# Optimization experiments

Measured on AMD Instinct MI355X. Metric: run time of the kernel, lower is better.

The kernel has to match this reference:

```python
import jax, jax.numpy as jnp
import numpy as np

BIG_NEG = -1e9


def setup_inputs() -> dict:
    key = jax.random.key(0)
    ks = jax.random.split(key, 6)
    b, N1, d, C1, K = 4, 511, 64, 31, 32
    features = jax.random.normal(ks[0], (b, N1, d), jnp.float32)
    transition_logits = jax.random.normal(ks[1], (C1, C1), jnp.float32)
    init_logits = jax.random.uniform(ks[2], (C1,), jnp.float32)
    poisson_log_rates = jax.random.normal(ks[3], (C1,), jnp.float32) * 0.5 + 1.5
    A = jax.random.normal(ks[5], (d, d), jnp.float32)
    gaussian_cov = jnp.eye(d, dtype=jnp.float32) + 0.1 * (A @ A.T) / d
    gaussian_means = jax.random.normal(ks[4], (C1, d), jnp.float32) * 0.1
    return {
        "features": features,
        "transition_logits": transition_logits,
        "init_logits": init_logits,
        "poisson_log_rates": poisson_log_rates,
        "gaussian_means": gaussian_means,
        "gaussian_cov": gaussian_cov,
        "max_k": K,
        "add_eos": 1,
    }


def reference(features, transition_logits, init_logits, poisson_log_rates,
              gaussian_means, gaussian_cov, max_k, add_eos):
    b, N1, d = features.shape
    C1 = transition_logits.shape[0]
    K = int(max_k)
    dt = features.dtype

    # transition log-probs: mask diagonal with BIG_NEG, normalize over axis 0 (torch dim=0)
    trans = jax.nn.log_softmax(
        jnp.where(jnp.eye(C1, dtype=bool), jnp.asarray(BIG_NEG, dt), transition_logits), axis=0)
    init = jax.nn.log_softmax(init_logits)

    # Poisson duration log-probs: k*log(rate) - rate - lgamma(k+1), k = 0..K-1
    rates = jnp.exp(poisson_log_rates)  # [C1]
    tsteps = jnp.arange(K, dtype=dt)[:, None]  # [K,1]
    length = tsteps * poisson_log_rates[None, :] - rates[None, :] - jax.scipy.special.gammaln(tsteps + 1.0)  # [K,C1]

    # Gaussian emission log-probs, shared full covariance across classes
    L = jnp.linalg.cholesky(gaussian_cov)
    Linv = jax.scipy.linalg.solve_triangular(L, jnp.eye(d, dtype=dt), lower=True)
    diff = features[:, :, None, :] - gaussian_means[None, None]          # [b,N1,C1,d]
    y = jnp.einsum('bncd,ed->bnce', diff, Linv)
    maha = jnp.sum(y * y, axis=-1)                                       # [b,N1,C1]
    logdet = 2.0 * jnp.sum(jnp.log(jnp.diag(L)))
    emis = -0.5 * (d * jnp.log(jnp.asarray(2.0 * jnp.pi, dt)) + logdet + maha)

    if add_eos:
        N, C = N1 + 1, C1 + 1
        trans_a = jnp.full((C, C), BIG_NEG, dt).at[:C1, :C1].set(trans).at[C1, :].set(0.0)
        init_a = jnp.full((C,), BIG_NEG, dt).at[:C1].set(init)
        length_a = jnp.full((K, C), BIG_NEG, dt).at[:, :C1].set(length).at[1, C1].set(0.0)
        emis_a = jnp.full((b, N, C), BIG_NEG, dt).at[:, :N1, :C1].set(emis).at[:, N1, C1].set(0.0)
    else:
        N, C = N1, C1
        trans_a, init_a, length_a, emis_a = trans, init, length, emis

    ep = jnp.pad(emis_a, ((0, 0), (0, K), (0, 0)))
    cs = jnp.concatenate([jnp.zeros((b, 1, C), dt), jnp.cumsum(ep, axis=1)], axis=1)  # [b,N+K+1,C]
    tt = jnp.arange(N - 1)[:, None]
    kk = jnp.arange(K)[None, :]
    win = cs[:, tt + kk] - cs[:, tt]  # [b, N-1, K, C]

    # edge scores: b x (N-1) x K x C_prev x C
    scores = (trans_a[None, None, None] +
              length_a[None, None, :, None, :] +
              win[:, :, :, None, :])
    scores = scores.at[:, 0].add(init_a[None, None, None, :])
    keos = jnp.arange(1, K)
    scores = scores.at[:, N - 1 - keos, keos].add(emis_a[:, N - 1][:, None, :, None])
    return scores
```

## Files before the change

kernel.cpp:

```cpp
#include <hip/hip_runtime.h>
#include <math.h>

#define BIG_NEG -1.0e9f

typedef float f4 __attribute__((ext_vector_type(4)));

constexpr int B  = 4;
constexpr int N1 = 511;
constexpr int C1 = 31;
constexpr int K  = 32;
constexpr int N  = N1 + 1;
constexpr int C  = C1 + 1;

constexpr int WS_TRANS = 0;
constexpr int WS_INIT  = 1024;
constexpr int WS_LEN   = 1056;
constexpr int WS_P     = 2080;
constexpr int WS_W     = 6176;
constexpr int WS_BIAS  = 8224;
constexpr int WS_EMIS  = 8256;

__global__ __launch_bounds__(512) void k_prep(const float* __restrict__ tl,
                                              const float* __restrict__ il,
                                              const float* __restrict__ plr,
                                              const float* __restrict__ cov,
                                              const float* __restrict__ means,
                                              float* __restrict__ ws) {
    __shared__ float M[64][132];
    __shared__ float cP[2][4][64];
    __shared__ float Bsave[16][16];
    __shared__ float mu[C1][64];

    const int tid = threadIdx.x;
    const int ii = tid >> 3;
    const int cg = tid & 7;

    f4* Mrow = (f4*)&M[ii][0];

    for (int idx = tid; idx < 1024; idx += 512) {
        const int i = idx >> 5, j = idx & 31;
        float lv;
        if (j < C1) {
            float lr = plr[j];
            lv = (float)i * lr - expf(lr) - lgammaf((float)i + 1.0f);
        } else {
            lv = (i == 1) ? 0.0f : BIG_NEG;
        }
        ws[WS_LEN + idx] = lv;
        if (i == C1) ws[WS_TRANS + idx] = 0.0f;
        else if (j == C1) ws[WS_TRANS + idx] = BIG_NEG;
    }
    if (tid < B * C) {
        const int bb = tid >> 5, cc = tid & 31;
        ws[WS_EMIS + (bb * N + N1) * C + cc] = (cc == C1) ? 0.0f : BIG_NEG;
    }
    if (tid < C1) {
        const int jj = tid;
        float m = BIG_NEG;
        for (int r = 0; r < C1; ++r) {
            float v = (r == jj) ? BIG_NEG : tl[r * C1 + jj];
            m = fmaxf(m, v);
        }
        float s = 0.0f;
        for (int r = 0; r < C1; ++r) {
            float v = (r == jj) ? BIG_NEG : tl[r * C1 + jj];
            s += expf(v - m);
        }
        float lse = m + logf(s);
        for (int r = 0; r < C1; ++r) {
            float v = (r == jj) ? BIG_NEG : tl[r * C1 + jj];
            ws[WS_TRANS + r * 32 + jj] = v - lse;
        }
    }
    if (tid == 32) {
        float m = -1.0e30f;
        for (int cc = 0; cc < C1; ++cc) m = fmaxf(m, il[cc]);
        float s = 0.0f;
        for (int cc = 0; cc < C1; ++cc) s += expf(il[cc] - m);
        float lse = m + logf(s);
        for (int cc = 0; cc < C1; ++cc) ws[WS_INIT + cc] = il[cc] - lse;
        ws[WS_INIT + C1] = BIG_NEG;
    }

    {
        Mrow[cg]     = *(const f4*)&cov[ii * 64 + 4 * cg];
        Mrow[cg + 8] = *(const f4*)&cov[ii * 64 + 4 * (cg + 8)];
        const int r0 = 4 * cg, r1 = 4 * (cg + 8);
        f4 e1 = {(ii == r0) ? 1.f : 0.f, (ii == r0 + 1) ? 1.f : 0.f,
                 (ii == r0 + 2) ? 1.f : 0.f, (ii == r0 + 3) ? 1.f : 0.f};
        f4 e2 = {(ii == r1) ? 1.f : 0.f, (ii == r1 + 1) ? 1.f : 0.f,
                 (ii == r1 + 2) ? 1.f : 0.f, (ii == r1 + 3) ? 1.f : 0.f};
        Mrow[cg + 16] = e1;
        Mrow[cg + 24] = e2;
    }
    if (cg == 0) {
        cP[0][0][ii] = cov[ii * 64 + 0];
        cP[0][1][ii] = cov[ii * 64 + 1];
        cP[0][2][ii] = cov[ii * 64 + 2];
        cP[0][3][ii] = cov[ii * 64 + 3];
    }
    for (int idx = tid; idx < C1 * 64; idx += 512)
        mu[idx >> 6][idx & 63] = means[idx];
    __syncthreads();

    float detprod = 1.0f;
    for (int st = 0; st < 16; ++st) {
        const int s = st << 2;
        const int par = st & 1;
        const float T00 = cP[par][0][s + 0], T01 = cP[par][0][s + 1],
                    T02 = cP[par][0][s + 2], T03 = cP[par][0][s + 3];
        const float T10 = cP[par][1][s + 0], T11 = cP[par][1][s + 1],
                    T12 = cP[par][1][s + 2], T13 = cP[par][1][s + 3];
        const float T20 = cP[par][2][s + 0], T21 = cP[par][2][s + 1],
                    T22 = cP[par][2][s + 2], T23 = cP[par][2][s + 3];
        const float T30 = cP[par][3][s + 0], T31 = cP[par][3][s + 1],
                    T32 = cP[par][3][s + 2], T33 = cP[par][3][s + 3];
        const float r0 = __builtin_amdgcn_rcpf(T00);
        const float l10 = T10 * r0, l20 = T20 * r0, l30 = T30 * r0;
        const float u11 = T11 - l10 * T01, u12 = T12 - l10 * T02,
                    u13 = T13 - l10 * T03;
        const float r1 = __builtin_amdgcn_rcpf(u11);
        const float l21 = (T21 - l20 * T01) * r1;
        const float l31 = (T31 - l30 * T01) * r1;
        const float u22 = T22 - l20 * T02 - l21 * u12;
        const float u23 = T23 - l20 * T03 - l21 * u13;
        const float u32 = T32 - l30 * T02 - l31 * u12;
        const float u33t = T33 - l30 * T03 - l31 * u13;
        const float r2 = __builtin_amdgcn_rcpf(u22);
        const float l32 = u32 * r2;
        const float u33 = u33t - l32 * u23;
        const float r3 = __builtin_amdgcn_rcpf(u33);
        detprod *= T00 * u11 * u22 * u33;

        if (tid < 16) Bsave[st][tid] = cP[par][tid & 3][s + (tid >> 2)];

        const float m0 = cP[par][0][ii], m1 = cP[par][1][ii],
                    m2 = cP[par][2][ii], m3 = cP[par][3][ii];
        const float y0 = m0;
        const float y1 = m1 - l10 * y0;
        const float y2 = m2 - l20 * y0 - l21 * y1;
        const float y3 = m3 - l30 * y0 - l31 * y1 - l32 * y2;
        float g3 = y3 * r3;
        float g2 = (y2 - u23 * g3) * r2;
        float g1 = (y1 - u12 * g2 - u13 * g3) * r1;
        float g0 = (y0 - T01 * g1 - T02 * g2 - T03 * g3) * r0;
        const bool pivrow = (unsigned)(ii - s) < 4u;
        if (pivrow) { g0 = 0.f; g1 = 0.f; g2 = 0.f; g3 = 0.f; }

        const f4* Ms0 = (const f4*)&M[s + 0][0];
        const f4* Ms1 = (const f4*)&M[s + 1][0];
        const f4* Ms2 = (const f4*)&M[s + 2][0];
        const f4* Ms3 = (const f4*)&M[s + 3][0];
        const int qpub = st + 1;
#pragma unroll
        for (int h = 0; h < 4; ++h) {
            const int q = cg + 8 * h;
            const int k0 = 4 * q;
            const bool active = (k0 < 64) ? (k0 + 3 >= s) : (k0 - 64 <= s + 3);
            if (!active) continue;
            f4 v = Mrow[q] - g0 * Ms0[q] - g1 * Ms1[q]
                           - g2 * Ms2[q] - g3 * Ms3[q];
            if (!pivrow) Mrow[q] = v;
            if (st < 15 && q == qpub) {
                cP[par ^ 1][0][ii] = v.x;
                cP[par ^ 1][1][ii] = v.y;
                cP[par ^ 1][2][ii] = v.z;
                cP[par ^ 1][3][ii] = v.w;
            }
        }
        __syncthreads();
    }

    {
        const int kb = ii >> 2, rsel = ii & 3, base = kb << 2;
        const float* Bk = &Bsave[kb][0];
        const float T00 = Bk[0],  T01 = Bk[4],  T02 = Bk[8],  T03 = Bk[12];
        const float T10 = Bk[1],  T11 = Bk[5],  T12 = Bk[9],  T13 = Bk[13];
        const float T20 = Bk[2],  T21 = Bk[6],  T22 = Bk[10], T23 = Bk[14];
        const float T30 = Bk[3],  T31 = Bk[7],  T32 = Bk[11], T33 = Bk[15];
        const float r0 = __builtin_amdgcn_rcpf(T00);
        const float l10 = T10 * r0, l20 = T20 * r0, l30 = T30 * r0;
        const float u11 = T11 - l10 * T01, u12 = T12 - l10 * T02,
                    u13 = T13 - l10 * T03;
        const float r1 = __builtin_amdgcn_rcpf(u11);
        const float l21 = (T21 - l20 * T01) * r1;
        const float l31 = (T31 - l30 * T01) * r1;
        const float u22 = T22 - l20 * T02 - l21 * u12;
        const float u23 = T23 - l20 * T03 - l21 * u13;
        const float u32 = T32 - l30 * T02 - l31 * u12;
        const float u33t = T33 - l30 * T03 - l31 * u13;
        const float r2 = __builtin_amdgcn_rcpf(u22);
        const float l32 = u32 * r2;
        const float u33 = u33t - l32 * u23;
        const float r3 = __builtin_amdgcn_rcpf(u33);
        const float m0 = (rsel == 0) ? 1.f : 0.f;
        const float m1 = (rsel == 1) ? 1.f : 0.f;
        const float m2 = (rsel == 2) ? 1.f : 0.f;
        const float m3 = (rsel == 3) ? 1.f : 0.f;
        const float y0 = m0;
        const float y1 = m1 - l10 * y0;
        const float y2 = m2 - l20 * y0 - l21 * y1;
        const float y3 = m3 - l30 * y0 - l31 * y1 - l32 * y2;
        const float x3 = y3 * r3;
        const float x2 = (y2 - u23 * x3) * r2;
        const float x1 = (y1 - u12 * x2 - u13 * x3) * r1;
        const float x0 = (y0 - T01 * x1 - T02 * x2 - T03 * x3) * r0;

        const f4* R0 = (const f4*)&M[base + 0][64];
        const f4* R1 = (const f4*)&M[base + 1][64];
        const f4* R2 = (const f4*)&M[base + 2][64];
        const f4* R3 = (const f4*)&M[base + 3][64];
        f4 va = x0 * R0[cg] + x1 * R1[cg] + x2 * R2[cg] + x3 * R3[cg];
        f4 vb = x0 * R0[cg + 8] + x1 * R1[cg + 8] +
                x2 * R2[cg + 8] + x3 * R3[cg + 8];
        *(f4*)&ws[WS_P + ii * 64 + 4 * cg] = va;
        *(f4*)&ws[WS_P + ii * 64 + 32 + 4 * cg] = vb;
        *(f4*)&M[ii][4 * cg] = va;
        *(f4*)&M[ii][32 + 4 * cg] = vb;
    }
    __syncthreads();

    {
        const int c = tid >> 4;
        const int l = tid & 15;
        if (c < C1) {
            const f4* muc = (const f4*)&mu[c][0];
            float qacc = 0.0f;
#pragma unroll
            for (int h = 0; h < 4; ++h) {
                const int dd = l + 16 * h;
                const f4* Mr = (const f4*)&M[dd][0];
                f4 a4 = {0.f, 0.f, 0.f, 0.f};
#pragma unroll
                for (int e4 = 0; e4 < 16; ++e4) a4 += Mr[e4] * muc[e4];
                float a = (a4.x + a4.y) + (a4.z + a4.w);
                ws[WS_W + dd * 32 + c] = a;
                qacc += a * mu[c][dd];
            }
            for (int m2 = 8; m2 >= 1; m2 >>= 1) qacc += __shfl_xor(qacc, m2, 64);
            if (l == 0)
                ws[WS_BIAS + c] = -0.5f * (64.0f * 1.8378770664093453f +
                                           logf(detprod) + qacc);
        }
    }
}

__global__ __launch_bounds__(256) void k_emis(const float* __restrict__ feat,
                                              float* __restrict__ ws) {
    const int tid = threadIdx.x;
    const int w = tid >> 6, lane = tid & 63;
    const int flat = blockIdx.x * 4 + w;
    const int b = flat / N1, n = flat % N1;
    __shared__ float xs[4][64];

    const float x = feat[flat * 64 + lane];
    xs[w][lane] = x;

    const float* __restrict__ P = ws + WS_P;
    float z = 0.0f;
    for (int dd = 0; dd < 64; ++dd) z += P[dd * 64 + lane] * xs[w][dd];

    float xz = x * z;
    for (int m = 32; m >= 1; m >>= 1) xz += __shfl_xor(xz, m);

    float val = BIG_NEG;
    if (lane < C1) {
        float s = ws[WS_BIAS + lane] - 0.5f * xz;
        const float* __restrict__ wT = ws + WS_W;
        for (int dd = 0; dd < 64; ++dd) s += wT[dd * 32 + lane] * xs[w][dd];
        val = s;
    }
    if (lane < C) ws[WS_EMIS + (b * N + n) * C + lane] = val;
}

__global__ __launch_bounds__(256) void k_main(const float* __restrict__ ws,
                                              float* __restrict__ out) {
    const int bid = blockIdx.x;
    const int b = bid / N1, t = bid % N1;
    const int tid = threadIdx.x;
    __shared__ float sh[32][36];

    {
        const int row = tid >> 3;
        const int c4 = (tid & 7) << 2;
        f4 v = {0.f, 0.f, 0.f, 0.f};
        if (t + row < N)
            v = *(const f4*)&ws[WS_EMIS + (b * N + t + row) * C + c4];
        *(f4*)&sh[row][c4] = v;
    }
    __syncthreads();

    {
        const int sc = tid >> 3;
        const int g  = tid & 7;
        float p0 = sh[4 * g + 0][sc];
        float p1 = p0 + sh[4 * g + 1][sc];
        float p2 = p1 + sh[4 * g + 2][sc];
        float p3 = p2 + sh[4 * g + 3][sc];
        float sum = p3;
#pragma unroll
        for (int off = 1; off < 8; off <<= 1) {
            float nv = __shfl_up(sum, off, 8);
            if (g >= off) sum += nv;
        }
        const float excl = sum - p3;
        sh[4 * g + 0][sc] = p0 + excl;
        sh[4 * g + 1][sc] = p1 + excl;
        sh[4 * g + 2][sc] = p2 + excl;
        sh[4 * g + 3][sc] = p3 + excl;
    }

    const int cp = tid >> 3;
    const int c0 = (tid & 7) << 2;
    f4 pre = *(const f4*)&ws[WS_TRANS + cp * 32 + c0];
    if (t == 0) {
        f4 in4 = *(const f4*)&ws[WS_INIT + c0];
        pre = pre + in4;
    }
    const float emisN = (cp == C1) ? 0.0f : BIG_NEG;
    const int keos = N1 - t;
    const size_t obase = (size_t)bid * (K * C * C) + (size_t)(cp * 32 + c0);
    __syncthreads();

#pragma unroll 4
    for (int k = 0; k < K; ++k) {
        f4 len4 = *(const f4*)&ws[WS_LEN + k * 32 + c0];
        f4 w4 = {0.f, 0.f, 0.f, 0.f};
        if (k > 0) w4 = *(const f4*)&sh[k - 1][c0];
        f4 o = pre + len4 + w4;
        if (k == keos) o = o + emisN;
        *(f4*)&out[obase + (size_t)k * (C * C)] = o;
    }
}

extern "C" void kernel_launch(void* const* d_in, const int* in_sizes, int n_in,
                              void* d_out, int out_size, void* d_ws, size_t ws_size,
                              hipStream_t stream) {
    const float* feat = (const float*)d_in[0];
    const float* tl   = (const float*)d_in[1];
    const float* il   = (const float*)d_in[2];
    const float* plr  = (const float*)d_in[3];
    const float* gm   = (const float*)d_in[4];
    const float* gc   = (const float*)d_in[5];
    float* ws  = (float*)d_ws;
    float* out = (float*)d_out;

    hipLaunchKernelGGL(k_prep, dim3(1), dim3(512), 0, stream, tl, il, plr, gc, gm, ws);
    hipLaunchKernelGGL(k_emis, dim3(B * N1 / 4), dim3(256), 0, stream, feat, ws);
    hipLaunchKernelGGL(k_main, dim3(B * N1), dim3(256), 0, stream, ws, out);
}
```

Baseline: 79.98 us.

## Fuse emission computation into main kernel with 8-timestep tiles per block

Drops the separate emission kernel and its workspace round trip. Each block now handles 8 consecutive timesteps: it loads the precision matrix and weights into shared memory, computes emissions for the 38 rows it needs, prefix-sums them, and writes the windowed score tensors for all 8 timesteps. This removes one launch and the global emission buffer, and amortizes the prefix scan across timesteps. In exchange it recomputes emissions for overlapping rows between blocks and shrinks the grid from 2044 to 256 blocks, which may reduce parallelism for the write-bound output phase.

Measured after the change: 88.11 us. +10.2%, slower.

```diff
diff --git a/kernel.cpp b/kernel.cpp
--- a/kernel.cpp
+++ b/kernel.cpp
@@ -18,7 +18,6 @@
 constexpr int WS_P     = 2080;
 constexpr int WS_W     = 6176;
 constexpr int WS_BIAS  = 8224;
-constexpr int WS_EMIS  = 8256;
 
 __global__ __launch_bounds__(512) void k_prep(const float* __restrict__ tl,
                                               const float* __restrict__ il,
@@ -49,10 +48,6 @@
         ws[WS_LEN + idx] = lv;
         if (i == C1) ws[WS_TRANS + idx] = 0.0f;
         else if (j == C1) ws[WS_TRANS + idx] = BIG_NEG;
-    }
-    if (tid < B * C) {
-        const int bb = tid >> 5, cc = tid & 31;
-        ws[WS_EMIS + (bb * N + N1) * C + cc] = (cc == C1) ? 0.0f : BIG_NEG;
     }
     if (tid < C1) {
         const int jj = tid;
@@ -245,91 +240,112 @@
     }
 }
 
-__global__ __launch_bounds__(256) void k_emis(const float* __restrict__ feat,
-                                              float* __restrict__ ws) {
+__global__ __launch_bounds__(256) void k_main(const float* __restrict__ feat,
+                                              const float* __restrict__ ws,
+                                              float* __restrict__ out) {
+    constexpr int TT = 8;
+    constexpr int ROWS = TT - 1 + 31;
+    const int bid = blockIdx.x;
+    const int b = bid >> 6;
+    const int t0 = (bid & 63) << 3;
     const int tid = threadIdx.x;
     const int w = tid >> 6, lane = tid & 63;
-    const int flat = blockIdx.x * 4 + w;
-    const int b = flat / N1, n = flat % N1;
-    __shared__ float xs[4][64];
-
-    const float x = feat[flat * 64 + lane];
-    xs[w][lane] = x;
-
-    const float* __restrict__ P = ws + WS_P;
-    float z = 0.0f;
-    for (int dd = 0; dd < 64; ++dd) z += P[dd * 64 + lane] * xs[w][dd];
-
-    float xz = x * z;
-    for (int m = 32; m >= 1; m >>= 1) xz += __shfl_xor(xz, m);
-
-    float val = BIG_NEG;
-    if (lane < C1) {
-        float s = ws[WS_BIAS + lane] - 0.5f * xz;
-        const float* __restrict__ wT = ws + WS_W;
-        for (int dd = 0; dd < 64; ++dd) s += wT[dd * 32 + lane] * xs[w][dd];
-        val = s;
-    }
-    if (lane < C) ws[WS_EMIS + (b * N + n) * C + lane] = val;
-}
-
-__global__ __launch_bounds__(256) void k_main(const float* __restrict__ ws,
-                                              float* __restrict__ out) {
-    const int bid = blockIdx.x;
-    const int b = bid / N1, t = bid % N1;
-    const int tid = threadIdx.x;
-    __shared__ float sh[32][36];
-
-    {
-        const int row = tid >> 3;
-        const int c4 = (tid & 7) << 2;
-        f4 v = {0.f, 0.f, 0.f, 0.f};
-        if (t + row < N)
-            v = *(const f4*)&ws[WS_EMIS + (b * N + t + row) * C + c4];
-        *(f4*)&sh[row][c4] = v;
+
+    __shared__ float sP[64][64];
+    __shared__ float sW[64][32];
+    __shared__ float sx[ROWS][64];
+    __shared__ float sh[ROWS + 3][36];
+    __shared__ float sb[32];
+
+    {
+        float* p = &sP[0][0];
+        for (int i = tid; i < 1024; i += 256)
+            *(f4*)&p[4 * i] = *(const f4*)&ws[WS_P + 4 * i];
+        float* q = &sW[0][0];
+        for (int i = tid; i < 512; i += 256)
+            *(f4*)&q[4 * i] = *(const f4*)&ws[WS_W + 4 * i];
+        if (tid < 32) { sb[tid] = ws[WS_BIAS + tid]; sh[0][tid] = 0.f; }
+        else if (tid < 64) sh[ROWS + 1][tid - 32] = 0.f;
+        else if (tid < 96) sh[ROWS + 2][tid - 64] = 0.f;
+        for (int idx = tid; idx < ROWS * 16; idx += 256) {
+            const int row = idx >> 4, c4 = (idx & 15) << 2;
+            const int n = t0 + row;
+            f4 v = {0.f, 0.f, 0.f, 0.f};
+            if (n < N1) v = *(const f4*)&feat[(b * N1 + n) * 64 + c4];
+            *(f4*)&sx[row][c4] = v;
+        }
+    }
+    __syncthreads();
+
+    const float bias_l = (lane < C1) ? sb[lane] : 0.f;
+    for (int r = w; r < ROWS; r += 4) {
+        const int n = t0 + r;
+        float val;
+        if (n < N1) {
+            const float xl = sx[r][lane];
+            float z = 0.f, wv = 0.f;
+            for (int dd = 0; dd < 64; ++dd) {
+                const float xd = sx[r][dd];
+                z  += sP[dd][lane] * xd;
+                wv += sW[dd][lane & 31] * xd;
+            }
+            float xz = xl * z;
+            for (int m2 = 32; m2 >= 1; m2 >>= 1) xz += __shfl_xor(xz, m2);
+            val = (lane < C1) ? (bias_l + wv - 0.5f * xz) : BIG_NEG;
+        } else if (n == N1) {
+            val = (lane == C1) ? 0.0f : BIG_NEG;
+        } else {
+            val = 0.0f;
+        }
+        if (lane < 32) sh[r + 1][lane] = val;
     }
     __syncthreads();
 
     {
         const int sc = tid >> 3;
         const int g  = tid & 7;
-        float p0 = sh[4 * g + 0][sc];
-        float p1 = p0 + sh[4 * g + 1][sc];
-        float p2 = p1 + sh[4 * g + 2][sc];
-        float p3 = p2 + sh[4 * g + 3][sc];
-        float sum = p3;
+        float p0 = sh[5 * g + 1][sc];
+        float p1 = p0 + sh[5 * g + 2][sc];
+        float p2 = p1 + sh[5 * g + 3][sc];
+        float p3 = p2 + sh[5 * g + 4][sc];
+        float p4 = p3 + sh[5 * g + 5][sc];
+        float sum = p4;
 #pragma unroll
         for (int off = 1; off < 8; off <<= 1) {
             float nv = __shfl_up(sum, off, 8);
             if (g >= off) sum += nv;
         }
-        const float excl = sum - p3;
-        sh[4 * g + 0][sc] = p0 + excl;
-        sh[4 * g + 1][sc] = p1 + excl;
-        sh[4 * g + 2][sc] = p2 + excl;
-        sh[4 * g + 3][sc] = p3 + excl;
-    }
+        const float excl = sum - p4;
+        sh[5 * g + 1][sc] = p0 + excl;
+        sh[5 * g + 2][sc] = p1 + excl;
+        sh[5 * g + 3][sc] = p2 + excl;
+        sh[5 * g + 4][sc] = p3 + excl;
+        sh[5 * g + 5][sc] = p4 + excl;
+    }
+    __syncthreads();
 
     const int cp = tid >> 3;
     const int c0 = (tid & 7) << 2;
-    f4 pre = *(const f4*)&ws[WS_TRANS + cp * 32 + c0];
-    if (t == 0) {
-        f4 in4 = *(const f4*)&ws[WS_INIT + c0];
-        pre = pre + in4;
-    }
+    const f4 tr4 = *(const f4*)&ws[WS_TRANS + cp * 32 + c0];
     const float emisN = (cp == C1) ? 0.0f : BIG_NEG;
-    const int keos = N1 - t;
-    const size_t obase = (size_t)bid * (K * C * C) + (size_t)(cp * 32 + c0);
-    __syncthreads();
-
+
+    for (int j = 0; j < TT; ++j) {
+        const int t = t0 + j;
+        if (t >= N1) break;
+        f4 base_j = tr4;
+        if (t == 0) base_j += *(const f4*)&ws[WS_INIT + c0];
+        const f4 Sj = *(const f4*)&sh[j][c0];
+        const int keos = N1 - t;
+        const size_t obase =
+            (size_t)(b * N1 + t) * 32768 + (size_t)(cp * 32 + c0);
 #pragma unroll 4
-    for (int k = 0; k < K; ++k) {
-        f4 len4 = *(const f4*)&ws[WS_LEN + k * 32 + c0];
-        f4 w4 = {0.f, 0.f, 0.f, 0.f};
-        if (k > 0) w4 = *(const f4*)&sh[k - 1][c0];
-        f4 o = pre + len4 + w4;
-        if (k == keos) o = o + emisN;
-        *(f4*)&out[obase + (size_t)k * (C * C)] = o;
+        for (int k = 0; k < K; ++k) {
+            const f4 len4 = *(const f4*)&ws[WS_LEN + k * 32 + c0];
+            const f4 win = *(const f4*)&sh[j + k][c0] - Sj;
+            f4 o = base_j + len4 + win;
+            if (k == keos) o += emisN;
+            *(f4*)&out[obase + (size_t)k * 1024] = o;
+        }
     }
 }
 
@@ -346,6 +362,5 @@
     float* out = (float*)d_out;
 
     hipLaunchKernelGGL(k_prep, dim3(1), dim3(512), 0, stream, tl, il, plr, gc, gm, ws);
-    hipLaunchKernelGGL(k_emis, dim3(B * N1 / 4), dim3(256), 0, stream, feat, ws);
-    hipLaunchKernelGGL(k_main, dim3(B * N1), dim3(256), 0, stream, ws, out);
+    hipLaunchKernelGGL(k_main, dim3(B * 64), dim3(256), 0, stream, feat, ws, out);
 }
```

## Process two time steps per block using shared prefix sums and cached length table

Applied to the files above, without the earlier changes.

Each k_main block now handles two consecutive time steps. It builds one inclusive prefix sum over 33 emission rows plus a zero row, and forms window sums as differences of prefix entries. The length table is staged into shared memory instead of being read from global memory on every k iteration. Halving the grid and reusing the loaded emission rows is meant to cut per-block setup and redundant global loads. The cost is a larger shared footprint and a slightly longer serial scan per block. The kernel is dominated by the output write, which is unchanged.

After: 79.57 us. About the same (-0.5%).

```diff
diff --git a/kernel.cpp b/kernel.cpp
--- a/kernel.cpp
+++ b/kernel.cpp
@@ -275,61 +275,82 @@
 
 __global__ __launch_bounds__(256) void k_main(const float* __restrict__ ws,
                                               float* __restrict__ out) {
+    constexpr int TT = 2;
+    constexpr int EROWS = TT - 1 + 31;
     const int bid = blockIdx.x;
-    const int b = bid / N1, t = bid % N1;
+    const int b = bid >> 8;
+    const int t0 = (bid & 255) << 1;
     const int tid = threadIdx.x;
-    __shared__ float sh[32][36];
-
-    {
-        const int row = tid >> 3;
-        const int c4 = (tid & 7) << 2;
+
+    __shared__ __align__(16) float slen[K * C];
+    __shared__ float sh[41][36];
+
+    for (int idx = tid; idx < K * C / 4; idx += 256)
+        *(f4*)&slen[4 * idx] = *(const f4*)&ws[WS_LEN + 4 * idx];
+
+    for (int idx = tid; idx < 33 * 8; idx += 256) {
+        const int r = idx >> 3, c4 = (idx & 7) << 2;
+        const int n = t0 + r;
         f4 v = {0.f, 0.f, 0.f, 0.f};
-        if (t + row < N)
-            v = *(const f4*)&ws[WS_EMIS + (b * N + t + row) * C + c4];
-        *(f4*)&sh[row][c4] = v;
-    }
+        if (n < N) v = *(const f4*)&ws[WS_EMIS + (b * N + n) * C + c4];
+        *(f4*)&sh[r + 1][c4] = v;
+    }
+    if (tid < 32) sh[0][tid] = 0.f;
+    if (tid >= 64 && tid < 288 - 32) {
+        const int z = tid - 64;
+        sh[34 + (z >> 5)][z & 31] = 0.f;
+    }
+    if (tid >= 224 && tid < 256) sh[40][tid - 224] = 0.f;
     __syncthreads();
 
     {
         const int sc = tid >> 3;
         const int g  = tid & 7;
-        float p0 = sh[4 * g + 0][sc];
-        float p1 = p0 + sh[4 * g + 1][sc];
-        float p2 = p1 + sh[4 * g + 2][sc];
-        float p3 = p2 + sh[4 * g + 3][sc];
-        float sum = p3;
+        float p0 = sh[5 * g + 1][sc];
+        float p1 = p0 + sh[5 * g + 2][sc];
+        float p2 = p1 + sh[5 * g + 3][sc];
+        float p3 = p2 + sh[5 * g + 4][sc];
+        float p4 = p3 + sh[5 * g + 5][sc];
+        float sum = p4;
 #pragma unroll
         for (int off = 1; off < 8; off <<= 1) {
             float nv = __shfl_up(sum, off, 8);
             if (g >= off) sum += nv;
         }
-        const float excl = sum - p3;
-        sh[4 * g + 0][sc] = p0 + excl;
-        sh[4 * g + 1][sc] = p1 + excl;
-        sh[4 * g + 2][sc] = p2 + excl;
-        sh[4 * g + 3][sc] = p3 + excl;
+        const float excl = sum - p4;
+        sh[5 * g + 1][sc] = p0 + excl;
+        sh[5 * g + 2][sc] = p1 + excl;
+        sh[5 * g + 3][sc] = p2 + excl;
+        sh[5 * g + 4][sc] = p3 + excl;
+        sh[5 * g + 5][sc] = p4 + excl;
     }
 
     const int cp = tid >> 3;
     const int c0 = (tid & 7) << 2;
-    f4 pre = *(const f4*)&ws[WS_TRANS + cp * 32 + c0];
-    if (t == 0) {
-        f4 in4 = *(const f4*)&ws[WS_INIT + c0];
-        pre = pre + in4;
-    }
+    const f4 tr4 = *(const f4*)&ws[WS_TRANS + cp * 32 + c0];
+    f4 in4 = {0.f, 0.f, 0.f, 0.f};
+    if (t0 == 0) in4 = *(const f4*)&ws[WS_INIT + c0];
     const float emisN = (cp == C1) ? 0.0f : BIG_NEG;
-    const int keos = N1 - t;
-    const size_t obase = (size_t)bid * (K * C * C) + (size_t)(cp * 32 + c0);
     __syncthreads();
 
+#pragma unroll
+    for (int j = 0; j < TT; ++j) {
+        const int t = t0 + j;
+        if (t >= N1) break;
+        f4 base_j = tr4;
+        if (t == 0) base_j += in4;
+        const f4 Sj = *(const f4*)&sh[j][c0];
+        const int keos = N1 - t;
+        const size_t obase =
+            (size_t)(b * N1 + t) * 32768 + (size_t)(cp * 32 + c0);
 #pragma unroll 4
-    for (int k = 0; k < K; ++k) {
-        f4 len4 = *(const f4*)&ws[WS_LEN + k * 32 + c0];
-        f4 w4 = {0.f, 0.f, 0.f, 0.f};
-        if (k > 0) w4 = *(const f4*)&sh[k - 1][c0];
-        f4 o = pre + len4 + w4;
-        if (k == keos) o = o + emisN;
-        *(f4*)&out[obase + (size_t)k * (C * C)] = o;
+        for (int k = 0; k < K; ++k) {
+            const f4 len4 = *(const f4*)&slen[k * 32 + c0];
+            const f4 win = *(const f4*)&sh[j + k][c0] - Sj;
+            f4 o = base_j + len4 + win;
+            if (k == keos) o += emisN;
+            *(f4*)&out[obase + (size_t)k * 1024] = o;
+        }
     }
 }
 
@@ -347,5 +368,5 @@
 
     hipLaunchKernelGGL(k_prep, dim3(1), dim3(512), 0, stream, tl, il, plr, gc, gm, ws);
     hipLaunchKernelGGL(k_emis, dim3(B * N1 / 4), dim3(256), 0, stream, feat, ws);
-    hipLaunchKernelGGL(k_main, dim3(B * N1), dim3(256), 0, stream, ws, out);
+    hipLaunchKernelGGL(k_main, dim3(B * 256), dim3(256), 0, stream, ws, out);
 }
```
